# Kernel optimization log

Measured on AMD Instinct MI355X. Metric: run time of the kernel, lower is better.

## Reference

```python
import jax, jax.numpy as jnp
import numpy as np

N_NODES = 50000
N_EDGES = 600000
N_GRAPHS = 256
D = 128
D_OUT = 32
NEG_SLOPE = 0.01
EPS = 1e-12


def setup_inputs() -> dict:
    key = jax.random.key(0)
    ks = jax.random.split(key, 10)
    x = jax.random.normal(ks[0], (N_NODES, D), dtype=jnp.float32)
    edge_index = jax.random.randint(ks[1], (2, N_EDGES), 0, N_NODES, dtype=jnp.int64)
    batch = jnp.sort(jax.random.randint(ks[2], (N_NODES,), 0, N_GRAPHS, dtype=jnp.int64))
    s = 1.0 / np.sqrt(D)
    return {
        "x": x,
        "edge_index": edge_index,
        "batch": batch,
        "W_fc1": jax.random.normal(ks[3], (D, D), dtype=jnp.float32) * s,
        "b_fc1": jnp.zeros((D,), dtype=jnp.float32),
        "W_gc1": jax.random.normal(ks[4], (D, D), dtype=jnp.float32) * s,
        "b_gc1": jnp.zeros((D,), dtype=jnp.float32),
        "W_gc2": jax.random.normal(ks[5], (D, D), dtype=jnp.float32) * s,
        "b_gc2": jnp.zeros((D,), dtype=jnp.float32),
        "W_fc2": jax.random.normal(ks[6], (D, D), dtype=jnp.float32) * s,
        "b_fc2": jnp.zeros((D,), dtype=jnp.float32),
        "W_fc3": jax.random.normal(ks[7], (D, D_OUT), dtype=jnp.float32) * s,
        "b_fc3": jnp.zeros((D_OUT,), dtype=jnp.float32),
    }


def _gcn_conv(h, src, dst, inv_sqrt_deg, inv_deg, W, b, n_nodes):
    # GCNConv with self-loops: out = D^{-1/2} (A+I) D^{-1/2} (h @ W) + b
    ht = h @ W  # [N, D]
    coef = inv_sqrt_deg[src] * inv_sqrt_deg[dst]  # [E]
    agg = jax.ops.segment_sum(ht[src] * coef[:, None], dst, num_segments=n_nodes)
    agg = agg + ht * inv_deg[:, None]  # self-loop term
    return agg + b


def reference(x, edge_index, batch, W_fc1, b_fc1, W_gc1, b_gc1, W_gc2, b_gc2,
              W_fc2, b_fc2, W_fc3, b_fc3):
    n = x.shape[0]
    src, dst = edge_index[0], edge_index[1]
    # degree with self-loops (in-degree over targets, unit edge weights)
    deg = jax.ops.segment_sum(jnp.ones_like(dst, dtype=x.dtype), dst, num_segments=n) + 1.0
    inv_sqrt_deg = jax.lax.rsqrt(deg)
    inv_deg = 1.0 / deg

    hx = x @ W_fc1 + b_fc1
    hx = jax.nn.leaky_relu(_gcn_conv(hx, src, dst, inv_sqrt_deg, inv_deg, W_gc1, b_gc1, n), NEG_SLOPE)
    hx = jax.nn.leaky_relu(_gcn_conv(hx, src, dst, inv_sqrt_deg, inv_deg, W_gc2, b_gc2, n), NEG_SLOPE)

    # global mean pool over graphs
    sums = jax.ops.segment_sum(hx, batch, num_segments=N_GRAPHS)  # [G, D]
    counts = jax.ops.segment_sum(jnp.ones((n,), dtype=x.dtype), batch, num_segments=N_GRAPHS)
    pooled = sums / jnp.maximum(counts, 1.0)[:, None]

    # L2 normalize (torch.nn.functional.normalize, p=2, dim=1)
    norm = jnp.sqrt(jnp.sum(pooled * pooled, axis=1, keepdims=True))
    hg = pooled / jnp.maximum(norm, EPS)

    h = jax.nn.leaky_relu(hg @ W_fc2 + b_fc2, NEG_SLOPE)
    out = h @ W_fc3 + b_fc3  # [G, D_OUT]
    return out
```

## Files before the change

kernel.cpp:

```cpp
#include <hip/hip_runtime.h>

#define N_NODES  50000
#define N_EDGES  600000
#define N_GRAPHS 256
#define DOUT     32
#define NEG      0.01f
#define SLOTS    64
#define PSLOTS   16
#define OSLOTS   48
#define GB_GEMM  391

typedef __attribute__((ext_vector_type(8))) short short8;
typedef __attribute__((ext_vector_type(4))) float f32x4;

__device__ __forceinline__ unsigned short bf16_rne(float x) {
    unsigned int u = __float_as_uint(x);
    return (unsigned short)((u + 0x7FFFu + ((u >> 16) & 1u)) >> 16);
}


__global__ __launch_bounds__(256) void k_pre(const float* __restrict__ W1,
                                             const float* __restrict__ b1,
                                             const float* __restrict__ W2,
                                             float* __restrict__ W12,
                                             float* __restrict__ b12,
                                             int* __restrict__ counts,
                                             const int* __restrict__ batch,
                                             int* __restrict__ gs,
                                             int* __restrict__ ge) {
    int bid = blockIdx.x;
    int tid = threadIdx.x;
    if (bid < 65) {
        int i = bid * 2 + (tid >> 7);
        int j = tid & 127;
        if (i < 129) {
            const float* left = (i < 128) ? (W1 + i * 128) : b1;
            float acc = 0.f;
#pragma unroll 4
            for (int k = 0; k < 128; ++k) acc += left[k] * W2[k * 128 + j];
            if (i < 128) W12[i * 128 + j] = acc;
            else b12[j] = acc;
        }
    } else if (bid < 261) {
        int i = (bid - 65) * 256 + tid;
        if (i < N_NODES) counts[i] = 0;
    } else {
        int i = (bid - 261) * 256 + tid;
        if (i < N_NODES) {
            int b = batch[i];
            if (i == 0 || batch[i - 1] != b) gs[b] = i;
            if (i == N_NODES - 1 || batch[i + 1] != b) ge[b] = i + 1;
        }
    }
}


__global__ __launch_bounds__(256) void k_fill_gemm(
    const int* __restrict__ src, const int* __restrict__ dst,
    int* __restrict__ counts, int* __restrict__ csrp, int* __restrict__ csro,
    const float* __restrict__ Xf, const float* __restrict__ Wsrc,
    const float* __restrict__ bias, unsigned short* __restrict__ Y, int n)
{
    __shared__ short Wl[16384];
    int bid = blockIdx.x;
    int tid = threadIdx.x;

    if (bid >= GB_GEMM) {
        int e = (bid - GB_GEMM) * 256 + tid;
        if (e < N_EDGES) {
            int s = src[e], d = dst[e];
            int slot = atomicAdd(&counts[d], 1);
            if (slot < PSLOTS) csrp[(d << 4) + slot] = s;
            else if (slot < SLOTS) csro[d * OSLOTS + slot - PSLOTS] = s;
        }
        return;
    }

    for (int idx = tid; idx < 16384; idx += 256) {
        float w = Wsrc[idx];
        int k = idx >> 7, c = idx & 127;
        int kt = k >> 5, nt = c >> 4;
        int lane = ((k & 31) >> 3) * 16 + (c & 15);
        int e = k & 7;
        Wl[((kt * 8 + nt) * 64 + lane) * 8 + e] = (short)bf16_rne(w);
    }
    __syncthreads();

    int wid = tid >> 6;
    int lane = tid & 63;
    int r0 = bid * 128 + wid * 32;
    int a0 = r0 + (lane & 15);      if (a0 >= n) a0 = n - 1;
    int a1 = r0 + 16 + (lane & 15); if (a1 >= n) a1 = n - 1;
    int ko = (lane >> 4) * 8;

    f32x4 acc0[8], acc1[8];
    f32x4 zero = {0.f, 0.f, 0.f, 0.f};
#pragma unroll
    for (int t = 0; t < 8; ++t) { acc0[t] = zero; acc1[t] = zero; }

#pragma unroll
    for (int kt = 0; kt < 4; ++kt) {
        int k0 = kt * 32 + ko;
        const float* p0 = Xf + (size_t)a0 * 128 + k0;
        const float* p1 = Xf + (size_t)a1 * 128 + k0;
        float4 u0 = *(const float4*)p0, u1 = *(const float4*)(p0 + 4);
        float4 v0 = *(const float4*)p1, v1 = *(const float4*)(p1 + 4);
        float us[8] = {u0.x, u0.y, u0.z, u0.w, u1.x, u1.y, u1.z, u1.w};
        float vs[8] = {v0.x, v0.y, v0.z, v0.w, v1.x, v1.y, v1.z, v1.w};
        short8 af0, af1;
#pragma unroll
        for (int i = 0; i < 8; ++i) {
            af0[i] = (short)bf16_rne(us[i]);
            af1[i] = (short)bf16_rne(vs[i]);
        }
#pragma unroll
        for (int t = 0; t < 8; ++t) {
            short8 bh = *(const short8*)&Wl[((kt * 8 + t) * 64 + lane) * 8];
            acc0[t] = __builtin_amdgcn_mfma_f32_16x16x32_bf16(af0, bh, acc0[t], 0, 0, 0);
            acc1[t] = __builtin_amdgcn_mfma_f32_16x16x32_bf16(af1, bh, acc1[t], 0, 0, 0);
        }
    }

    int rbase = r0 + (lane >> 4) * 4;
    int col0 = lane & 15;
#pragma unroll
    for (int t = 0; t < 8; ++t) {
        int col = t * 16 + col0;
        float badd = bias[col];
#pragma unroll
        for (int r = 0; r < 4; ++r) {
            int row0 = rbase + r;
            int row1 = rbase + 16 + r;
            if (row0 < n) Y[(size_t)row0 * 128 + col] = bf16_rne(acc0[t][r] + badd);
            if (row1 < n) Y[(size_t)row1 * 128 + col] = bf16_rne(acc1[t][r] + badd);
        }
    }
}


__global__ __launch_bounds__(256) void k_gemm_mfma(
    const unsigned short* __restrict__ Xh, const float* __restrict__ Wsrc,
    unsigned short* __restrict__ Y, int n)
{
    __shared__ short Wl[16384];
    int tid = threadIdx.x;
    for (int idx = tid; idx < 16384; idx += 256) {
        float w = Wsrc[idx];
        int k = idx >> 7, c = idx & 127;
        int kt = k >> 5, nt = c >> 4;
        int lane = ((k & 31) >> 3) * 16 + (c & 15);
        int e = k & 7;
        Wl[((kt * 8 + nt) * 64 + lane) * 8 + e] = (short)bf16_rne(w);
    }
    __syncthreads();

    int wid = tid >> 6;
    int lane = tid & 63;
    int r0 = blockIdx.x * 128 + wid * 32;
    int a0 = r0 + (lane & 15);      if (a0 >= n) a0 = n - 1;
    int a1 = r0 + 16 + (lane & 15); if (a1 >= n) a1 = n - 1;
    int ko = (lane >> 4) * 8;

    f32x4 acc0[8], acc1[8];
    f32x4 zero = {0.f, 0.f, 0.f, 0.f};
#pragma unroll
    for (int t = 0; t < 8; ++t) { acc0[t] = zero; acc1[t] = zero; }

#pragma unroll
    for (int kt = 0; kt < 4; ++kt) {
        int k0 = kt * 32 + ko;
        short8 af0 = *(const short8*)(Xh + (size_t)a0 * 128 + k0);
        short8 af1 = *(const short8*)(Xh + (size_t)a1 * 128 + k0);
#pragma unroll
        for (int t = 0; t < 8; ++t) {
            short8 bh = *(const short8*)&Wl[((kt * 8 + t) * 64 + lane) * 8];
            acc0[t] = __builtin_amdgcn_mfma_f32_16x16x32_bf16(af0, bh, acc0[t], 0, 0, 0);
            acc1[t] = __builtin_amdgcn_mfma_f32_16x16x32_bf16(af1, bh, acc1[t], 0, 0, 0);
        }
    }

    int rbase = r0 + (lane >> 4) * 4;
    int col0 = lane & 15;
#pragma unroll
    for (int t = 0; t < 8; ++t) {
        int col = t * 16 + col0;
#pragma unroll
        for (int r = 0; r < 4; ++r) {
            int row0 = rbase + r;
            int row1 = rbase + 16 + r;
            if (row0 < n) Y[(size_t)row0 * 128 + col] = bf16_rne(acc0[t][r]);
            if (row1 < n) Y[(size_t)row1 * 128 + col] = bf16_rne(acc1[t][r]);
        }
    }
}


__global__ __launch_bounds__(256) void k_agg(const unsigned short* __restrict__ HT,
                                             const int* __restrict__ csrp,
                                             const int* __restrict__ csro,
                                             const int* __restrict__ counts,
                                             const float* __restrict__ bias,
                                             unsigned short* __restrict__ OUT, int n) {
    int node = blockIdx.x * 4 + (threadIdx.x >> 6);
    int lane = threadIdx.x & 63;
    if (node >= n) return;
    const unsigned int* H = (const unsigned int*)HT;
    int deg = counts[node];
    float is = rsqrtf((float)deg + 1.0f);
    int c1 = deg < PSLOTS ? deg : PSLOTS;
    int base = node << 4;

    unsigned int su = H[(size_t)node * 64 + lane];
    float2 b = ((const float2*)bias)[lane];

    float acc0 = 0.f, acc1 = 0.f, acc2 = 0.f, acc3 = 0.f;
    int j = 0;
    for (; j + 8 <= c1; j += 8) {
        int sx[8];
#pragma unroll
        for (int q = 0; q < 8; ++q) sx[q] = csrp[base + j + q];
        int dg[8];
#pragma unroll
        for (int q = 0; q < 8; ++q) dg[q] = counts[sx[q]];
        unsigned int v[8];
#pragma unroll
        for (int q = 0; q < 8; ++q) v[q] = H[(size_t)sx[q] * 64 + lane];
#pragma unroll
        for (int q = 0; q < 8; ++q) {
            float c = rsqrtf((float)dg[q] + 1.0f) * is;
            float f0 = __uint_as_float(v[q] << 16);
            float f1 = __uint_as_float(v[q] & 0xFFFF0000u);
            if (q & 1) { acc2 += f0 * c; acc3 += f1 * c; }
            else       { acc0 += f0 * c; acc1 += f1 * c; }
        }
    }
    for (; j + 4 <= c1; j += 4) {
        int sx[4];
#pragma unroll
        for (int q = 0; q < 4; ++q) sx[q] = csrp[base + j + q];
        int dg[4];
#pragma unroll
        for (int q = 0; q < 4; ++q) dg[q] = counts[sx[q]];
        unsigned int v[4];
#pragma unroll
        for (int q = 0; q < 4; ++q) v[q] = H[(size_t)sx[q] * 64 + lane];
#pragma unroll
        for (int q = 0; q < 4; ++q) {
            float c = rsqrtf((float)dg[q] + 1.0f) * is;
            float f0 = __uint_as_float(v[q] << 16);
            float f1 = __uint_as_float(v[q] & 0xFFFF0000u);
            if (q & 1) { acc2 += f0 * c; acc3 += f1 * c; }
            else       { acc0 += f0 * c; acc1 += f1 * c; }
        }
    }
    for (; j < c1; ++j) {
        int s = csrp[base + j];
        float c = rsqrtf((float)counts[s] + 1.0f) * is;
        unsigned int v = H[(size_t)s * 64 + lane];
        acc0 += __uint_as_float(v << 16) * c;
        acc1 += __uint_as_float(v & 0xFFFF0000u) * c;
    }
    int c2 = deg < SLOTS ? deg : SLOTS;
    for (j = PSLOTS; j < c2; ++j) {
        int s = csro[node * OSLOTS + j - PSLOTS];
        float c = rsqrtf((float)counts[s] + 1.0f) * is;
        unsigned int v = H[(size_t)s * 64 + lane];
        acc0 += __uint_as_float(v << 16) * c;
        acc1 += __uint_as_float(v & 0xFFFF0000u) * c;
    }

    float invd = is * is;
    float sv0 = __uint_as_float(su << 16);
    float sv1 = __uint_as_float(su & 0xFFFF0000u);
    float ox = acc0 + acc2 + sv0 * invd + b.x;
    float oy = acc1 + acc3 + sv1 * invd + b.y;
    ox = ox > 0.f ? ox : ox * NEG;
    oy = oy > 0.f ? oy : oy * NEG;
    unsigned int pk = (unsigned int)bf16_rne(ox) | ((unsigned int)bf16_rne(oy) << 16);
    ((unsigned int*)OUT)[(size_t)node * 64 + lane] = pk;
}


__global__ __launch_bounds__(256) void k_pool_final(const unsigned short* __restrict__ Hn,
                                                    const int* __restrict__ gs,
                                                    const int* __restrict__ ge,
                                                    const float* __restrict__ W2,
                                                    const float* __restrict__ b2,
                                                    const float* __restrict__ W3,
                                                    const float* __restrict__ b3,
                                                    float* __restrict__ out) {
    __shared__ float part[4][128];
    __shared__ float red[128];
    __shared__ float h1[128];
    int g = blockIdx.x, tid = threadIdx.x;
    int c2 = tid & 63, rr = tid >> 6;
    int s = gs[g], e = ge[g];
    const unsigned int* H = (const unsigned int*)Hn;
    float2 acc = make_float2(0.f, 0.f);
    for (int r = s + rr; r < e; r += 4) {
        unsigned int v = H[(size_t)r * 64 + c2];
        acc.x += __uint_as_float(v << 16);
        acc.y += __uint_as_float(v & 0xFFFF0000u);
    }
    part[rr][c2 * 2] = acc.x;
    part[rr][c2 * 2 + 1] = acc.y;
    __syncthreads();
    float mean = 0.f;
    if (tid < 128) {
        mean = (part[0][tid] + part[1][tid] + part[2][tid] + part[3][tid])
               / fmaxf((float)(e - s), 1.f);
        red[tid] = mean * mean;
    }
    __syncthreads();
    for (int off = 64; off > 0; off >>= 1) {
        if (tid < off) red[tid] += red[tid + off];
        __syncthreads();
    }
    if (tid < 128) {
        float norm = sqrtf(red[0]);
        part[0][tid] = mean / fmaxf(norm, 1e-12f);
    }
    __syncthreads();
    if (tid < 128) {
        float a = b2[tid];
#pragma unroll 8
        for (int k = 0; k < 128; ++k) a += part[0][k] * W2[k * 128 + tid];
        a = a > 0.f ? a : a * NEG;
        h1[tid] = a;
    }
    __syncthreads();
    if (tid < DOUT) {
        float a2 = b3[tid];
#pragma unroll 8
        for (int k = 0; k < 128; ++k) a2 += h1[k] * W3[k * DOUT + tid];
        out[g * DOUT + tid] = a2;
    }
}


extern "C" void kernel_launch(void* const* d_in, const int* in_sizes, int n_in,
                              void* d_out, int out_size, void* d_ws, size_t ws_size,
                              hipStream_t stream) {
    const float* x      = (const float*)d_in[0];
    const int*   ei     = (const int*)d_in[1];
    const int*   batch  = (const int*)d_in[2];
    const float* W_fc1  = (const float*)d_in[3];
    const float* b_fc1  = (const float*)d_in[4];
    const float* W_gc1  = (const float*)d_in[5];
    const float* b_gc1  = (const float*)d_in[6];
    const float* W_gc2  = (const float*)d_in[7];
    const float* b_gc2  = (const float*)d_in[8];
    const float* W_fc2  = (const float*)d_in[9];
    const float* b_fc2  = (const float*)d_in[10];
    const float* W_fc3  = (const float*)d_in[11];
    const float* b_fc3  = (const float*)d_in[12];
    float* out = (float*)d_out;

    const int N = N_NODES, E = N_EDGES;
    const int* e_src = ei;
    const int* e_dst = ei + E;

    char* ws = (char*)d_ws;
    unsigned short* H0     = (unsigned short*)(ws + 0);
    unsigned short* H1     = (unsigned short*)(ws + 12800000);
    int*            csrp   = (int*)  (ws + 25600000);
    int*            csro   = (int*)  (ws + 28800000);
    int*            counts = (int*)  (ws + 38400000);
    int*            gs     = (int*)  (ws + 38600000);
    int*            ge     = (int*)  (ws + 38601024);
    float*          W12    = (float*)(ws + 38602048);
    float*          b12    = (float*)(ws + 38667584);

    const int EB = (E + 255) / 256;

    k_pre<<<457, 256, 0, stream>>>(W_fc1, b_fc1, W_gc1, W12, b12, counts, batch, gs, ge);
    k_fill_gemm<<<GB_GEMM + EB, 256, 0, stream>>>(e_src, e_dst, counts, csrp, csro,
                                                  x, W12, b12, H1, N);
    k_agg<<<(N + 3) / 4, 256, 0, stream>>>(H1, csrp, csro, counts, b_gc1, H0, N);
    k_gemm_mfma<<<GB_GEMM, 256, 0, stream>>>(H0, W_gc2, H1, N);
    k_agg<<<(N + 3) / 4, 256, 0, stream>>>(H1, csrp, csro, counts, b_gc2, H0, N);
    k_pool_final<<<N_GRAPHS, 256, 0, stream>>>(H0, gs, ge, W_fc2, b_fc2, W_fc3, b_fc3, out);

    (void)in_sizes; (void)n_in; (void)out_size; (void)ws_size;
}
```

Measured before the change: 157.1 us.

## Store CSR neighbor indices as 16-bit and widen primary slot array

Neighbor indices in the per-node slot arrays are stored as unsigned short instead of int, halving index traffic in the fill and aggregation kernels. The primary slot count grows from 16 to 32 so more neighbors hit the unrolled fast path, and the overflow array shrinks to 32 slots. Nontemporal loads and stores are added for edge reads, the fp32 input in the fused GEMM, and its bf16 output. Node indices go up to 50000, which fits in 16 bits, but this ties correctness to the node count staying below 65536.

```diff
diff --git a/kernel.cpp b/kernel.cpp
--- a/kernel.cpp
+++ b/kernel.cpp
@@ -6,8 +6,7 @@
 #define DOUT     32
 #define NEG      0.01f
 #define SLOTS    64
-#define PSLOTS   16
-#define OSLOTS   48
+#define PSLOTS   32
 #define GB_GEMM  391
 
 typedef __attribute__((ext_vector_type(8))) short short8;
@@ -57,7 +56,8 @@
 
 __global__ __launch_bounds__(256) void k_fill_gemm(
     const int* __restrict__ src, const int* __restrict__ dst,
-    int* __restrict__ counts, int* __restrict__ csrp, int* __restrict__ csro,
+    int* __restrict__ counts,
+    unsigned short* __restrict__ csrp, unsigned short* __restrict__ csro,
     const float* __restrict__ Xf, const float* __restrict__ Wsrc,
     const float* __restrict__ bias, unsigned short* __restrict__ Y, int n)
 {
@@ -68,10 +68,11 @@
     if (bid >= GB_GEMM) {
         int e = (bid - GB_GEMM) * 256 + tid;
         if (e < N_EDGES) {
-            int s = src[e], d = dst[e];
+            int d = __builtin_nontemporal_load(&dst[e]);
+            int s = __builtin_nontemporal_load(&src[e]);
             int slot = atomicAdd(&counts[d], 1);
-            if (slot < PSLOTS) csrp[(d << 4) + slot] = s;
-            else if (slot < SLOTS) csro[d * OSLOTS + slot - PSLOTS] = s;
+            if (slot < PSLOTS) csrp[(d << 5) + slot] = (unsigned short)s;
+            else if (slot < SLOTS) csro[(d << 5) + slot - PSLOTS] = (unsigned short)s;
         }
         return;
     }
@@ -103,15 +104,17 @@
         int k0 = kt * 32 + ko;
         const float* p0 = Xf + (size_t)a0 * 128 + k0;
         const float* p1 = Xf + (size_t)a1 * 128 + k0;
-        float4 u0 = *(const float4*)p0, u1 = *(const float4*)(p0 + 4);
-        float4 v0 = *(const float4*)p1, v1 = *(const float4*)(p1 + 4);
-        float us[8] = {u0.x, u0.y, u0.z, u0.w, u1.x, u1.y, u1.z, u1.w};
-        float vs[8] = {v0.x, v0.y, v0.z, v0.w, v1.x, v1.y, v1.z, v1.w};
+        f32x4 u0 = __builtin_nontemporal_load((const f32x4*)p0);
+        f32x4 u1 = __builtin_nontemporal_load((const f32x4*)(p0 + 4));
+        f32x4 v0 = __builtin_nontemporal_load((const f32x4*)p1);
+        f32x4 v1 = __builtin_nontemporal_load((const f32x4*)(p1 + 4));
         short8 af0, af1;
 #pragma unroll
-        for (int i = 0; i < 8; ++i) {
-            af0[i] = (short)bf16_rne(us[i]);
-            af1[i] = (short)bf16_rne(vs[i]);
+        for (int i = 0; i < 4; ++i) {
+            af0[i]     = (short)bf16_rne(u0[i]);
+            af0[i + 4] = (short)bf16_rne(u1[i]);
+            af1[i]     = (short)bf16_rne(v0[i]);
+            af1[i + 4] = (short)bf16_rne(v1[i]);
         }
 #pragma unroll
         for (int t = 0; t < 8; ++t) {
@@ -131,8 +134,12 @@
         for (int r = 0; r < 4; ++r) {
             int row0 = rbase + r;
             int row1 = rbase + 16 + r;
-            if (row0 < n) Y[(size_t)row0 * 128 + col] = bf16_rne(acc0[t][r] + badd);
-            if (row1 < n) Y[(size_t)row1 * 128 + col] = bf16_rne(acc1[t][r] + badd);
+            if (row0 < n)
+                __builtin_nontemporal_store(bf16_rne(acc0[t][r] + badd),
+                                            &Y[(size_t)row0 * 128 + col]);
+            if (row1 < n)
+                __builtin_nontemporal_store(bf16_rne(acc1[t][r] + badd),
+                                            &Y[(size_t)row1 * 128 + col]);
         }
     }
 }
@@ -196,8 +203,8 @@
 
 
 __global__ __launch_bounds__(256) void k_agg(const unsigned short* __restrict__ HT,
-                                             const int* __restrict__ csrp,
-                                             const int* __restrict__ csro,
+                                             const unsigned short* __restrict__ csrp,
+                                             const unsigned short* __restrict__ csro,
                                              const int* __restrict__ counts,
                                              const float* __restrict__ bias,
                                              unsigned short* __restrict__ OUT, int n) {
@@ -208,7 +215,7 @@
     int deg = counts[node];
     float is = rsqrtf((float)deg + 1.0f);
     int c1 = deg < PSLOTS ? deg : PSLOTS;
-    int base = node << 4;
+    int base = node << 5;
 
     unsigned int su = H[(size_t)node * 64 + lane];
     float2 b = ((const float2*)bias)[lane];
@@ -262,7 +269,7 @@
     }
     int c2 = deg < SLOTS ? deg : SLOTS;
     for (j = PSLOTS; j < c2; ++j) {
-        int s = csro[node * OSLOTS + j - PSLOTS];
+        int s = csro[base + j - PSLOTS];
         float c = rsqrtf((float)counts[s] + 1.0f) * is;
         unsigned int v = H[(size_t)s * 64 + lane];
         acc0 += __uint_as_float(v << 16) * c;
@@ -356,22 +363,22 @@
     const float* b_fc3  = (const float*)d_in[12];
     float* out = (float*)d_out;
 
-    const int N = N_NODES, E = N_EDGES;
+    const int N = N_NODES;
     const int* e_src = ei;
-    const int* e_dst = ei + E;
+    const int* e_dst = ei + N_EDGES;
 
     char* ws = (char*)d_ws;
     unsigned short* H0     = (unsigned short*)(ws + 0);
     unsigned short* H1     = (unsigned short*)(ws + 12800000);
-    int*            csrp   = (int*)  (ws + 25600000);
-    int*            csro   = (int*)  (ws + 28800000);
-    int*            counts = (int*)  (ws + 38400000);
-    int*            gs     = (int*)  (ws + 38600000);
-    int*            ge     = (int*)  (ws + 38601024);
-    float*          W12    = (float*)(ws + 38602048);
-    float*          b12    = (float*)(ws + 38667584);
-
-    const int EB = (E + 255) / 256;
+    unsigned short* csrp   = (unsigned short*)(ws + 25600000);
+    unsigned short* csro   = (unsigned short*)(ws + 28800000);
+    int*            counts = (int*)  (ws + 32000000);
+    int*            gs     = (int*)  (ws + 32200000);
+    int*            ge     = (int*)  (ws + 32201024);
+    float*          W12    = (float*)(ws + 32202048);
+    float*          b12    = (float*)(ws + 32267584);
+
+    const int EB = (N_EDGES + 255) / 256;
 
     k_pre<<<457, 256, 0, stream>>>(W_fc1, b_fc1, W_gc1, W12, b12, counts, batch, gs, ge);
     k_fill_gemm<<<GB_GEMM + EB, 256, 0, stream>>>(e_src, e_dst, counts, csrp, csro,
```

New measurement: 157.2 us. Within noise of the previous version (+0.1%).
